# Optimization experiments

Hardware: AMD Instinct MI355X
Metric: run time of the kernel (lower is better)

## Reference

```python
import jax, jax.numpy as jnp
import numpy as np

EPSILON = 1e-19
MASKING_RATIO = 0.75
N_BINS = 64
SIGMA = 0.01


def setup_inputs() -> dict:
    key = jax.random.key(0)
    k1, k2 = jax.random.split(key)
    N, L, D = 4, 512, 1024
    P = 768  # 16*16*3 pixels per patch
    x = jax.random.normal(k1, (N, L, D), dtype=jnp.float32)
    img_pat = jax.random.uniform(k2, (N, L, P), dtype=jnp.float32)
    return {"x": x, "img_pat": img_pat}


def _entropy_kde(values, n_bins=N_BINS, sigma=SIGMA):
    # values: [N, L, P]; global min/max normalization as in the torch code
    bins = jnp.linspace(0.0, 1.0, n_bins, dtype=values.dtype)  # [B]
    vmin = values.min()
    vmax = values.max()
    nv = (values - vmin) / (vmax - vmin)
    # residuals: [N, L, B, P]
    resid = nv[:, :, None, :] - bins[None, None, :, None]
    kern = jnp.exp(-0.5 * (resid / sigma) ** 2)
    pdf = kern.mean(axis=3)  # [N, L, B]
    pdf = pdf / (pdf.sum(axis=2, keepdims=True) + EPSILON) + EPSILON
    return -jnp.sum(pdf * jnp.log(pdf), axis=-1)  # [N, L]


def reference(x, img_pat):
    # entropy_kde_masking branch of MaskingModule.forward
    N, L, D = x.shape
    len_keep = int(L * (1.0 - MASKING_RATIO))
    entropies = _entropy_kde(img_pat)                 # [N, L]
    ids_shuffle = jnp.argsort(entropies, axis=1)      # ascending (descending=False)
    ids_restore = jnp.argsort(ids_shuffle, axis=1)    # [N, L]
    ids_keep = ids_shuffle[:, :len_keep]              # [N, len_keep]
    x_masked = jnp.take_along_axis(x, ids_keep[:, :, None], axis=1)  # [N, len_keep, D]
    mask = jnp.ones((N, L), dtype=x.dtype).at[:, :len_keep].set(0.0)
    mask = jnp.take_along_axis(mask, ids_restore, axis=1)
    return (x_masked, mask, ids_restore)
```

## Files before the change

kernel.cpp:

```cpp
#include <hip/hip_runtime.h>

#define NB 4
#define LB 512
#define DB 1024
#define PB 768
#define NBINS 64
#define LEN_KEEP 128
#define EPSL 1e-19f
#define WIN 3

#if defined(__has_builtin)
#if __has_builtin(__builtin_amdgcn_exp2f)
#define HAVE_EXP2 1
#endif
#endif

__device__ __forceinline__ float fast_exp2(float x) {
#ifdef HAVE_EXP2
    return __builtin_amdgcn_exp2f(x);
#else
    return __expf(x * 0.69314718055994530942f);
#endif
}

__global__ void minmax_partial(const float4* __restrict__ v,
                               float* __restrict__ bmin, float* __restrict__ bmax) {
    __shared__ float smin[256], smax[256];
    int tid = threadIdx.x;
    int base = blockIdx.x * 256 + tid;
    float mn = 1e30f, mx = -1e30f;
#pragma unroll
    for (int k = 0; k < 24; ++k) {
        float4 t4 = v[base + k * 16384];
        mn = fminf(mn, fminf(fminf(t4.x, t4.y), fminf(t4.z, t4.w)));
        mx = fmaxf(mx, fmaxf(fmaxf(t4.x, t4.y), fmaxf(t4.z, t4.w)));
    }
    smin[tid] = mn; smax[tid] = mx;
    __syncthreads();
    for (int s = 128; s > 0; s >>= 1) {
        if (tid < s) {
            smin[tid] = fminf(smin[tid], smin[tid + s]);
            smax[tid] = fmaxf(smax[tid], smax[tid + s]);
        }
        __syncthreads();
    }
    if (tid == 0) { bmin[blockIdx.x] = smin[0]; bmax[blockIdx.x] = smax[0]; }
}

__global__ void entropy_kernel(const float* __restrict__ img,
                               const float* __restrict__ bmin,
                               const float* __restrict__ bmax,
                               float* __restrict__ ent) {
    __shared__ float sh[256];
    __shared__ float snv[PB];
    __shared__ int   cnt[NBINS];
    __shared__ int   bs[NBINS + 1];
    __shared__ int   pos[NBINS];

    int t = blockIdx.x;
    int tid = threadIdx.x;
    int lane = tid & 63;
    int w = tid >> 6;

    if (tid < NBINS) cnt[tid] = 0;
    if (tid < 64) {
        float mn = bmin[tid], mx = bmax[tid];
        for (int m = 1; m < 64; m <<= 1) {
            mn = fminf(mn, __shfl_xor(mn, m, 64));
            mx = fmaxf(mx, __shfl_xor(mx, m, 64));
        }
        if (tid == 0) { sh[0] = mn; sh[1] = mx; }
    }
    __syncthreads();
    float vmin = sh[0], vmax = sh[1];
    float inv = 1.0f / (vmax - vmin);

    const float* row = img + (size_t)t * PB;
    float nv0 = (row[tid]       - vmin) * inv;
    float nv1 = (row[tid + 256] - vmin) * inv;
    float nv2 = (row[tid + 512] - vmin) * inv;
    int m0 = min(63, max(0, __float2int_rn(nv0 * 63.0f)));
    int m1 = min(63, max(0, __float2int_rn(nv1 * 63.0f)));
    int m2 = min(63, max(0, __float2int_rn(nv2 * 63.0f)));
    atomicAdd(&cnt[m0], 1);
    atomicAdd(&cnt[m1], 1);
    atomicAdd(&cnt[m2], 1);
    __syncthreads();

    if (tid < 64) {
        int c = cnt[tid];
        int incl = c;
        for (int off = 1; off < 64; off <<= 1) {
            int up = __shfl_up(incl, off, 64);
            if (tid >= off) incl += up;
        }
        bs[tid + 1] = incl;
        pos[tid] = incl - c;
        if (tid == 0) bs[0] = 0;
    }
    __syncthreads();

    snv[atomicAdd(&pos[m0], 1)] = nv0;
    snv[atomicAdd(&pos[m1], 1)] = nv1;
    snv[atomicAdd(&pos[m2], 1)] = nv2;
    __syncthreads();

    float bv = (float)lane * (1.0f / 63.0f);
    int lo = bs[max(0, lane - WIN)];
    int hi = bs[min(NBINS, lane + WIN + 1)];
    const float negC = -7213.4755859375f;
    float acc = 0.0f;
    for (int j = lo + w; j < hi; j += 4) {
        float d = snv[j] - bv;
        acc += fast_exp2(d * d * negC);
    }
    sh[w * NBINS + lane] = acc;
    __syncthreads();

    if (tid < 64) {
        float pdf = (sh[lane] + sh[64 + lane] + sh[128 + lane] + sh[192 + lane])
                    * (1.0f / (float)PB);
        float s = pdf;
        for (int m = 1; m < 64; m <<= 1) s += __shfl_xor(s, m, 64);
        float p = pdf / (s + EPSL) + EPSL;
        float term = p * __logf(p);
        for (int m = 1; m < 64; m <<= 1) term += __shfl_xor(term, m, 64);
        if (tid == 0) ent[t] = -term;
    }
}

__global__ void rank_gather_kernel(const float* __restrict__ x,
                                   const float* __restrict__ ent,
                                   float* __restrict__ out_x,
                                   float* __restrict__ out_mask,
                                   float* __restrict__ out_rest) {
    __shared__ float sh[LB];
    __shared__ int keep_list[16];
    __shared__ int nkeep;
    int b = blockIdx.x, tid = threadIdx.x;
    int n = b >> 5;
    int i = (b & 31) * 16 + (tid >> 4);
    int slice = tid & 15;

    if (tid == 0) nkeep = 0;
    sh[tid]       = ent[n * LB + tid];
    sh[256 + tid] = ent[n * LB + 256 + tid];
    __syncthreads();

    unsigned long long ci =
        ((unsigned long long)__float_as_uint(sh[i]) << 32) | (unsigned int)i;
    int r = 0;
    int j0 = slice * 32;
#pragma unroll 8
    for (int j = j0; j < j0 + 32; ++j) {
        unsigned long long cj =
            ((unsigned long long)__float_as_uint(sh[j]) << 32) | (unsigned int)j;
        r += (cj < ci) ? 1 : 0;
    }
    r += __shfl_xor(r, 1, 64);
    r += __shfl_xor(r, 2, 64);
    r += __shfl_xor(r, 4, 64);
    r += __shfl_xor(r, 8, 64);
    if (slice == 0) {
        out_rest[n * LB + i] = (float)r;
        out_mask[n * LB + i] = (r < LEN_KEEP) ? 0.0f : 1.0f;
        if (r < LEN_KEEP) {
            int e = atomicAdd(&nkeep, 1);
            keep_list[e] = (r << 16) | i;
        }
    }
    __syncthreads();

    int nk = nkeep;
    for (int e = 0; e < nk; ++e) {
        int ent_ri = keep_list[e];
        int slot = ent_ri >> 16;
        int rowi = ent_ri & 0xFFFF;
        const float4* src = (const float4*)(x + ((size_t)(n * LB + rowi)) * DB);
        float4* dst = (float4*)(out_x + ((size_t)(n * LEN_KEEP + slot)) * DB);
        dst[tid] = src[tid];
    }
}

extern "C" void kernel_launch(void* const* d_in, const int* in_sizes, int n_in,
                              void* d_out, int out_size, void* d_ws, size_t ws_size,
                              hipStream_t stream) {
    const float* x   = (const float*)d_in[0];
    const float* img = (const float*)d_in[1];

    float* out      = (float*)d_out;
    float* out_x    = out;
    float* out_mask = out + (size_t)NB * LEN_KEEP * DB;
    float* out_rest = out_mask + NB * LB;

    float* ws   = (float*)d_ws;
    float* bmin = ws;
    float* bmax = ws + 64;
    float* ent  = ws + 128;

    minmax_partial<<<64, 256, 0, stream>>>((const float4*)img, bmin, bmax);
    entropy_kernel<<<NB * LB, 256, 0, stream>>>(img, bmin, bmax, ent);
    rank_gather_kernel<<<128, 256, 0, stream>>>(x, ent, out_x, out_mask, out_rest);
}
```

Measured before the change: 76.53 us.

## Fuse minmax, entropy and rank-gather into one cooperative kernel with grid syncs

Replaces three kernel launches with a single cooperative kernel of 512 blocks that uses grid-wide syncs between the min/max reduction, the per-patch KDE entropy and the rank/gather stages. The entropy stage now gives each wavefront its own patch with private LDS, so block-level barriers become wave-local waits and the per-bin window loop runs in a single wave. The rank stage assigns one row per wave instead of sixteen threads per row. The aim is to remove launch overhead and barrier cost, at the price of two grid barriers and a fixed grid size that must be fully co-resident.

```diff
diff --git a/kernel.cpp b/kernel.cpp
--- a/kernel.cpp
+++ b/kernel.cpp
@@ -1,4 +1,7 @@
 #include <hip/hip_runtime.h>
+#include <hip/hip_cooperative_groups.h>
+
+namespace cg = cooperative_groups;
 
 #define NB 4
 #define LB 512
@@ -8,6 +11,8 @@
 #define LEN_KEEP 128
 #define EPSL 1e-19f
 #define WIN 3
+#define NBLK 512
+#define NTHR 256
 
 #if defined(__has_builtin)
 #if __has_builtin(__builtin_amdgcn_exp2f)
@@ -23,162 +28,156 @@
 #endif
 }
 
-__global__ void minmax_partial(const float4* __restrict__ v,
-                               float* __restrict__ bmin, float* __restrict__ bmax) {
-    __shared__ float smin[256], smax[256];
-    int tid = threadIdx.x;
-    int base = blockIdx.x * 256 + tid;
-    float mn = 1e30f, mx = -1e30f;
-#pragma unroll
-    for (int k = 0; k < 24; ++k) {
-        float4 t4 = v[base + k * 16384];
-        mn = fminf(mn, fminf(fminf(t4.x, t4.y), fminf(t4.z, t4.w)));
-        mx = fmaxf(mx, fmaxf(fmaxf(t4.x, t4.y), fmaxf(t4.z, t4.w)));
-    }
-    smin[tid] = mn; smax[tid] = mx;
-    __syncthreads();
-    for (int s = 128; s > 0; s >>= 1) {
-        if (tid < s) {
-            smin[tid] = fminf(smin[tid], smin[tid + s]);
-            smax[tid] = fmaxf(smax[tid], smax[tid + s]);
-        }
-        __syncthreads();
-    }
-    if (tid == 0) { bmin[blockIdx.x] = smin[0]; bmax[blockIdx.x] = smax[0]; }
-}
-
-__global__ void entropy_kernel(const float* __restrict__ img,
-                               const float* __restrict__ bmin,
-                               const float* __restrict__ bmax,
-                               float* __restrict__ ent) {
-    __shared__ float sh[256];
-    __shared__ float snv[PB];
-    __shared__ int   cnt[NBINS];
-    __shared__ int   bs[NBINS + 1];
-    __shared__ int   pos[NBINS];
-
-    int t = blockIdx.x;
-    int tid = threadIdx.x;
-    int lane = tid & 63;
-    int w = tid >> 6;
-
-    if (tid < NBINS) cnt[tid] = 0;
-    if (tid < 64) {
-        float mn = bmin[tid], mx = bmax[tid];
+__global__ __launch_bounds__(NTHR, 2) void fused_kernel(
+        const float* __restrict__ x, const float* __restrict__ img,
+        float* __restrict__ out_x, float* __restrict__ out_mask,
+        float* __restrict__ out_rest,
+        float* __restrict__ bminp, float* __restrict__ bmaxp,
+        float* __restrict__ ent)
+{
+    __shared__ float lds[4 * 896];
+    __shared__ float shred[8];
+    __shared__ int keep_list[16];
+    __shared__ int nkeep;
+
+    const int tid = threadIdx.x;
+    const int bid = blockIdx.x;
+    const int lane = tid & 63;
+    const int w = tid >> 6;
+
+    {
+        const float4* v4 = (const float4*)img;
+        int g = bid * NTHR + tid;
+        float mn = 1e30f, mx = -1e30f;
+#pragma unroll
+        for (int k = 0; k < 3; ++k) {
+            float4 t4 = v4[g + k * (NBLK * NTHR)];
+            mn = fminf(mn, fminf(fminf(t4.x, t4.y), fminf(t4.z, t4.w)));
+            mx = fmaxf(mx, fmaxf(fmaxf(t4.x, t4.y), fmaxf(t4.z, t4.w)));
+        }
         for (int m = 1; m < 64; m <<= 1) {
             mn = fminf(mn, __shfl_xor(mn, m, 64));
             mx = fmaxf(mx, __shfl_xor(mx, m, 64));
         }
-        if (tid == 0) { sh[0] = mn; sh[1] = mx; }
+        if (lane == 0) { shred[w] = mn; shred[4 + w] = mx; }
+        __syncthreads();
+        if (tid == 0) {
+            bminp[bid] = fminf(fminf(shred[0], shred[1]), fminf(shred[2], shred[3]));
+            bmaxp[bid] = fmaxf(fmaxf(shred[4], shred[5]), fmaxf(shred[6], shred[7]));
+        }
     }
-    __syncthreads();
-    float vmin = sh[0], vmax = sh[1];
-    float inv = 1.0f / (vmax - vmin);
-
-    const float* row = img + (size_t)t * PB;
-    float nv0 = (row[tid]       - vmin) * inv;
-    float nv1 = (row[tid + 256] - vmin) * inv;
-    float nv2 = (row[tid + 512] - vmin) * inv;
-    int m0 = min(63, max(0, __float2int_rn(nv0 * 63.0f)));
-    int m1 = min(63, max(0, __float2int_rn(nv1 * 63.0f)));
-    int m2 = min(63, max(0, __float2int_rn(nv2 * 63.0f)));
-    atomicAdd(&cnt[m0], 1);
-    atomicAdd(&cnt[m1], 1);
-    atomicAdd(&cnt[m2], 1);
-    __syncthreads();
-
-    if (tid < 64) {
-        int c = cnt[tid];
-        int incl = c;
+    cg::this_grid().sync();
+
+    {
+        float mn = 1e30f, mx = -1e30f;
+#pragma unroll
+        for (int k = 0; k < 8; ++k) {
+            mn = fminf(mn, bminp[lane + 64 * k]);
+            mx = fmaxf(mx, bmaxp[lane + 64 * k]);
+        }
+        for (int m = 1; m < 64; m <<= 1) {
+            mn = fminf(mn, __shfl_xor(mn, m, 64));
+            mx = fmaxf(mx, __shfl_xor(mx, m, 64));
+        }
+        const float vmin = mn;
+        const float inv = 1.0f / (mx - mn);
+
+        const int t = bid * 4 + w;
+        float* snv = lds + w * 896;
+        int*   cnt = (int*)(snv + 768);
+        int*   pos = (int*)(snv + 832);
+
+        cnt[lane] = 0;
+        asm volatile("s_waitcnt lgkmcnt(0)" ::: "memory");
+
+        const float4* row4 = (const float4*)(img + (size_t)t * PB);
+        float4 a = row4[lane], b = row4[lane + 64], c = row4[lane + 128];
+        float nv[12] = { a.x, a.y, a.z, a.w, b.x, b.y, b.z, b.w,
+                         c.x, c.y, c.z, c.w };
+        int mb[12];
+#pragma unroll
+        for (int k = 0; k < 12; ++k) {
+            nv[k] = (nv[k] - vmin) * inv;
+            mb[k] = min(63, max(0, __float2int_rn(nv[k] * 63.0f)));
+            atomicAdd(&cnt[mb[k]], 1);
+        }
+        asm volatile("s_waitcnt lgkmcnt(0)" ::: "memory");
+
+        int c0 = cnt[lane];
+        int incl = c0;
         for (int off = 1; off < 64; off <<= 1) {
             int up = __shfl_up(incl, off, 64);
-            if (tid >= off) incl += up;
-        }
-        bs[tid + 1] = incl;
-        pos[tid] = incl - c;
-        if (tid == 0) bs[0] = 0;
-    }
-    __syncthreads();
-
-    snv[atomicAdd(&pos[m0], 1)] = nv0;
-    snv[atomicAdd(&pos[m1], 1)] = nv1;
-    snv[atomicAdd(&pos[m2], 1)] = nv2;
-    __syncthreads();
-
-    float bv = (float)lane * (1.0f / 63.0f);
-    int lo = bs[max(0, lane - WIN)];
-    int hi = bs[min(NBINS, lane + WIN + 1)];
-    const float negC = -7213.4755859375f;
-    float acc = 0.0f;
-    for (int j = lo + w; j < hi; j += 4) {
-        float d = snv[j] - bv;
-        acc += fast_exp2(d * d * negC);
-    }
-    sh[w * NBINS + lane] = acc;
-    __syncthreads();
-
-    if (tid < 64) {
-        float pdf = (sh[lane] + sh[64 + lane] + sh[128 + lane] + sh[192 + lane])
-                    * (1.0f / (float)PB);
+            if (lane >= off) incl += up;
+        }
+        pos[lane] = incl - c0;
+        int lov = __shfl(incl, max(lane - (WIN + 1), 0), 64);
+        int lo = (lane >= WIN + 1) ? lov : 0;
+        int hi = __shfl(incl, min(lane + WIN, 63), 64);
+        asm volatile("s_waitcnt lgkmcnt(0)" ::: "memory");
+
+#pragma unroll
+        for (int k = 0; k < 12; ++k) {
+            snv[atomicAdd(&pos[mb[k]], 1)] = nv[k];
+        }
+        asm volatile("s_waitcnt lgkmcnt(0)" ::: "memory");
+
+        const float bv = (float)lane * (1.0f / 63.0f);
+        const float negC = -7213.4755859375f;
+        float acc = 0.0f;
+        for (int j = lo; j < hi; ++j) {
+            float d = snv[j] - bv;
+            acc += fast_exp2(d * d * negC);
+        }
+
+        float pdf = acc * (1.0f / (float)PB);
         float s = pdf;
         for (int m = 1; m < 64; m <<= 1) s += __shfl_xor(s, m, 64);
         float p = pdf / (s + EPSL) + EPSL;
         float term = p * __logf(p);
         for (int m = 1; m < 64; m <<= 1) term += __shfl_xor(term, m, 64);
-        if (tid == 0) ent[t] = -term;
+        if (lane == 0) ent[t] = -term;
     }
-}
-
-__global__ void rank_gather_kernel(const float* __restrict__ x,
-                                   const float* __restrict__ ent,
-                                   float* __restrict__ out_x,
-                                   float* __restrict__ out_mask,
-                                   float* __restrict__ out_rest) {
-    __shared__ float sh[LB];
-    __shared__ int keep_list[16];
-    __shared__ int nkeep;
-    int b = blockIdx.x, tid = threadIdx.x;
-    int n = b >> 5;
-    int i = (b & 31) * 16 + (tid >> 4);
-    int slice = tid & 15;
-
-    if (tid == 0) nkeep = 0;
-    sh[tid]       = ent[n * LB + tid];
-    sh[256 + tid] = ent[n * LB + 256 + tid];
-    __syncthreads();
-
-    unsigned long long ci =
-        ((unsigned long long)__float_as_uint(sh[i]) << 32) | (unsigned int)i;
-    int r = 0;
-    int j0 = slice * 32;
-#pragma unroll 8
-    for (int j = j0; j < j0 + 32; ++j) {
-        unsigned long long cj =
-            ((unsigned long long)__float_as_uint(sh[j]) << 32) | (unsigned int)j;
-        r += (cj < ci) ? 1 : 0;
-    }
-    r += __shfl_xor(r, 1, 64);
-    r += __shfl_xor(r, 2, 64);
-    r += __shfl_xor(r, 4, 64);
-    r += __shfl_xor(r, 8, 64);
-    if (slice == 0) {
-        out_rest[n * LB + i] = (float)r;
-        out_mask[n * LB + i] = (r < LEN_KEEP) ? 0.0f : 1.0f;
-        if (r < LEN_KEEP) {
-            int e = atomicAdd(&nkeep, 1);
-            keep_list[e] = (r << 16) | i;
-        }
-    }
-    __syncthreads();
-
-    int nk = nkeep;
-    for (int e = 0; e < nk; ++e) {
-        int ent_ri = keep_list[e];
-        int slot = ent_ri >> 16;
-        int rowi = ent_ri & 0xFFFF;
-        const float4* src = (const float4*)(x + ((size_t)(n * LB + rowi)) * DB);
-        float4* dst = (float4*)(out_x + ((size_t)(n * LEN_KEEP + slot)) * DB);
-        dst[tid] = src[tid];
+    cg::this_grid().sync();
+
+    {
+        const int n = bid >> 7;
+        const int ibase = (bid & 127) * 4;
+        float* sh = lds;
+        if (tid == 0) nkeep = 0;
+        sh[tid]       = ent[n * LB + tid];
+        sh[256 + tid] = ent[n * LB + 256 + tid];
+        __syncthreads();
+
+        const int i = ibase + w;
+        unsigned long long ci =
+            ((unsigned long long)__float_as_uint(sh[i]) << 32) | (unsigned)i;
+        int r = 0;
+#pragma unroll
+        for (int k = 0; k < 8; ++k) {
+            int j = lane + 64 * k;
+            unsigned long long cj =
+                ((unsigned long long)__float_as_uint(sh[j]) << 32) | (unsigned)j;
+            r += (cj < ci) ? 1 : 0;
+        }
+        for (int m = 1; m < 64; m <<= 1) r += __shfl_xor(r, m, 64);
+        if (lane == 0) {
+            out_rest[n * LB + i] = (float)r;
+            out_mask[n * LB + i] = (r < LEN_KEEP) ? 0.0f : 1.0f;
+            if (r < LEN_KEEP) {
+                int e = atomicAdd(&nkeep, 1);
+                keep_list[e] = (r << 16) | i;
+            }
+        }
+        __syncthreads();
+
+        const int nk = nkeep;
+        for (int e = 0; e < nk; ++e) {
+            int slot = keep_list[e] >> 16;
+            int rowi = keep_list[e] & 0xFFFF;
+            const float4* src = (const float4*)(x + ((size_t)(n * LB + rowi)) * DB);
+            float4* dst = (float4*)(out_x + ((size_t)(n * LEN_KEEP + slot)) * DB);
+            dst[tid] = src[tid];
+        }
     }
 }
 
@@ -193,12 +192,13 @@
     float* out_mask = out + (size_t)NB * LEN_KEEP * DB;
     float* out_rest = out_mask + NB * LB;
 
-    float* ws   = (float*)d_ws;
-    float* bmin = ws;
-    float* bmax = ws + 64;
-    float* ent  = ws + 128;
-
-    minmax_partial<<<64, 256, 0, stream>>>((const float4*)img, bmin, bmax);
-    entropy_kernel<<<NB * LB, 256, 0, stream>>>(img, bmin, bmax, ent);
-    rank_gather_kernel<<<128, 256, 0, stream>>>(x, ent, out_x, out_mask, out_rest);
+    float* ws    = (float*)d_ws;
+    float* bminp = ws;
+    float* bmaxp = ws + 512;
+    float* ent   = ws + 1024;
+
+    void* args[] = { (void*)&x, (void*)&img, (void*)&out_x, (void*)&out_mask,
+                     (void*)&out_rest, (void*)&bminp, (void*)&bmaxp, (void*)&ent };
+    hipLaunchCooperativeKernel((const void*)fused_kernel, dim3(NBLK), dim3(NTHR),
+                               args, 0, stream);
 }
```

Result: slower. 173.2 us (+126.4%).
